# Optimization experiments

Hardware: AMD Instinct MI355X
Metric: run time of the kernel (lower is better)

## Reference

```python
import jax, jax.numpy as jnp
import numpy as np
import math

FEATURE_DIM = 512
QK_DIM = 256
EPS = 1e-12  # torch F.normalize eps


def _l2norm(x):
    n = jnp.linalg.norm(x, axis=-1, keepdims=True)
    return x / jnp.maximum(n, EPS)


def setup_inputs() -> dict:
    key = jax.random.key(0)
    ks = jax.random.split(key, 6)
    B, Nq, Nk = 16, 2048, 2048
    query = jax.random.normal(ks[0], (B, Nq, FEATURE_DIM), dtype=jnp.float32)
    key_t = jax.random.normal(ks[1], (B, Nk, FEATURE_DIM // 2), dtype=jnp.float32)
    value = jax.random.normal(ks[2], (B, Nk, FEATURE_DIM // 2), dtype=jnp.float32)
    # weights stored torch-style [out, in], init N(0, sqrt(2/out))
    WQ = jax.random.normal(ks[3], (QK_DIM, FEATURE_DIM), dtype=jnp.float32) * math.sqrt(2.0 / QK_DIM)
    WK = jax.random.normal(ks[4], (QK_DIM, FEATURE_DIM // 2), dtype=jnp.float32) * math.sqrt(2.0 / QK_DIM)
    WV = jax.random.normal(ks[5], (FEATURE_DIM, FEATURE_DIM // 2), dtype=jnp.float32) * math.sqrt(2.0 / FEATURE_DIM)
    return {"query": query, "key": key_t, "value": value, "WQ": WQ, "WK": WK, "WV": WV}


def reference(query, key, value, WQ, WK, WV):
    temp = QK_DIM ** (-0.5)
    w_q = _l2norm(jnp.einsum('bnf,qf->bnq', query, WQ))      # [B, Nq, D]
    w_k = _l2norm(jnp.einsum('bmf,qf->bmq', key, WK))        # [B, Nk, D]
    dot = jnp.einsum('bnd,bmd->bnm', w_q, w_k)               # cosine sims
    affinity = jax.nn.softmax(dot * temp, axis=-1)
    w_v = _l2norm(jnp.einsum('bmf,vf->bmv', value, WV))      # [B, Nk, F]
    out = jnp.einsum('bnm,bmv->bnv', affinity, w_v)
    return out + query
```

## Files before the change

### kernel.cpp

```cpp
#include <hip/hip_runtime.h>

typedef float        f32x4  __attribute__((ext_vector_type(4)));
typedef float        f32x16 __attribute__((ext_vector_type(16)));
typedef unsigned int u32x4  __attribute__((ext_vector_type(4)));
typedef unsigned int u32x2  __attribute__((ext_vector_type(2)));
typedef int          i32x2  __attribute__((ext_vector_type(2)));
typedef __bf16       bf16x8 __attribute__((ext_vector_type(8)));

#define DEVFN static __device__ __forceinline__

DEVFN unsigned cvtpk(float a, float b){
  unsigned r;
  asm("v_cvt_pk_bf16_f32 %0, %1, %2" : "=v"(r) : "v"(a), "v"(b));
  return r;
}
DEVFN float exp2_hw(float x){
  float r;
  asm("v_exp_f32 %0, %1" : "=v"(r) : "v"(x));
  return r;
}
DEVFN bf16x8 as_bf(u32x4 v){ union{u32x4 u; bf16x8 b;} x; x.u=v; return x.b; }

DEVFN unsigned char f2fp8(float v){
  int r = __builtin_amdgcn_cvt_pk_fp8_f32(v, v, 0, false);
  return (unsigned char)(r & 0xff);
}
DEVFN unsigned pk4_fp8(float a, float b, float c, float d){
  int r = __builtin_amdgcn_cvt_pk_fp8_f32(a, b, 0, false);
  r = __builtin_amdgcn_cvt_pk_fp8_f32(c, d, r, true);
  return (unsigned)r;
}
DEVFN long mk64(unsigned lo, unsigned hi){
  return (long)(((unsigned long long)hi << 32) | lo);
}

DEVFN void plswap(unsigned &x, unsigned &y, int h){
#if __has_builtin(__builtin_amdgcn_permlane32_swap)
  i32x2 r = __builtin_amdgcn_permlane32_swap((int)x, (int)y, false, false);
  x = (unsigned)r[0]; y = (unsigned)r[1];
#else
  unsigned ox = (unsigned)__shfl_xor((int)x, 32);
  unsigned oy = (unsigned)__shfl_xor((int)y, 32);
  unsigned nx = h ? oy : x;
  unsigned ny = h ? y  : ox;
  x = nx; y = ny;
#endif
}

DEVFN void gload16(const char* src, char* lds){
  __builtin_amdgcn_global_load_lds(
      (__attribute__((address_space(1))) void*)src,
      (__attribute__((address_space(3))) void*)lds, 16, 0, 0);
}

constexpr int BB = 16, NQ = 2048, NK = 2048, F = 512, D = 256, FV = 512;

template<int KD, int ND, int MODE>
__global__ __launch_bounds__(256,2) void proj_kernel(const float* __restrict__ X,
                                                     const float* __restrict__ W,
                                                     unsigned char* __restrict__ Y,
                                                     float scale)
{
  constexpr bool TR = (MODE == 2);
  constexpr int NW = ND/4;
  constexpr int AF = TR ? 8 : 2;
  constexpr int BF = TR ? 2 : NW/16;
  __shared__ __align__(16) char xsm[32*80];
  __shared__ __align__(16) char wsm[ND*80];
  __shared__ float wsum[4][32];
  const int tid = threadIdx.x;
  const int lane = tid & 63;
  const int wid = tid >> 6;
  const int q16 = lane & 15;
  const int g = lane >> 4;
  const int row0 = blockIdx.x * 32;
  const int rX = tid >> 3, cX = (tid & 7) * 4;

  f32x4 z4 = {0.f,0.f,0.f,0.f};
  f32x4 acc[AF][BF];
  #pragma unroll
  for (int i=0;i<AF;i++){
    #pragma unroll
    for (int j=0;j<BF;j++) acc[i][j] = z4;
  }

  f32x4 xr = *(const f32x4*)(X + (size_t)(row0+rX)*KD + cX);
  f32x4 wr[ND/32];
  #pragma unroll
  for (int j=0;j<ND/32;j++)
    wr[j] = *(const f32x4*)(W + (size_t)(j*32+rX)*KD + cX);

  for (int k0 = 0; k0 < KD; k0 += 32){
    {
      u32x2 p; p[0]=cvtpk(xr[0],xr[1]); p[1]=cvtpk(xr[2],xr[3]);
      *(u32x2*)(xsm + rX*80 + cX*2) = p;
    }
    #pragma unroll
    for (int j=0;j<ND/32;j++){
      u32x2 p; p[0]=cvtpk(wr[j][0],wr[j][1]); p[1]=cvtpk(wr[j][2],wr[j][3]);
      *(u32x2*)(wsm + (j*32+rX)*80 + cX*2) = p;
    }
    if (k0 + 32 < KD){
      xr = *(const f32x4*)(X + (size_t)(row0+rX)*KD + k0+32 + cX);
      #pragma unroll
      for (int j=0;j<ND/32;j++)
        wr[j] = *(const f32x4*)(W + (size_t)(j*32+rX)*KD + k0+32 + cX);
    }
    __syncthreads();
    if constexpr (!TR){
      bf16x8 a[2], bb[BF];
      #pragma unroll
      for (int mi=0;mi<2;mi++)  a[mi]  = as_bf(*(const u32x4*)(xsm + (16*mi+q16)*80 + g*16));
      #pragma unroll
      for (int ni=0;ni<BF;ni++) bb[ni] = as_bf(*(const u32x4*)(wsm + (wid*NW + 16*ni + q16)*80 + g*16));
      #pragma unroll
      for (int mi=0;mi<2;mi++){
        #pragma unroll
        for (int ni=0;ni<BF;ni++)
          acc[mi][ni] = __builtin_amdgcn_mfma_f32_16x16x32_bf16(a[mi], bb[ni], acc[mi][ni], 0,0,0);
      }
    } else {
      bf16x8 a[8], bb[2];
      #pragma unroll
      for (int ai=0;ai<8;ai++) a[ai] = as_bf(*(const u32x4*)(wsm + (wid*NW + 16*ai + q16)*80 + g*16));
      #pragma unroll
      for (int ci=0;ci<2;ci++) bb[ci] = as_bf(*(const u32x4*)(xsm + (16*ci+q16)*80 + g*16));
      #pragma unroll
      for (int ai=0;ai<8;ai++){
        #pragma unroll
        for (int ci=0;ci<2;ci++)
          acc[ai][ci] = __builtin_amdgcn_mfma_f32_16x16x32_bf16(a[ai], bb[ci], acc[ai][ci], 0,0,0);
      }
    }
    __syncthreads();
  }

  if constexpr (!TR){
    float part[2][4];
    #pragma unroll
    for (int mi=0;mi<2;mi++){
      #pragma unroll
      for (int r=0;r<4;r++){
        float s=0.f;
        #pragma unroll
        for (int ni=0;ni<BF;ni++){ float v=acc[mi][ni][r]; s += v*v; }
        part[mi][r]=s;
      }
    }
    #pragma unroll
    for (int m=1;m<16;m<<=1){
      #pragma unroll
      for (int mi=0;mi<2;mi++){
        #pragma unroll
        for (int r=0;r<4;r++) part[mi][r] += __shfl_xor(part[mi][r], m);
      }
    }
    if (q16 == 0){
      #pragma unroll
      for (int mi=0;mi<2;mi++){
        #pragma unroll
        for (int r=0;r<4;r++) wsum[wid][16*mi + 4*g + r] = part[mi][r];
      }
    }
    __syncthreads();
    #pragma unroll
    for (int mi=0;mi<2;mi++){
      #pragma unroll
      for (int r=0;r<4;r++){
        int m = 16*mi + 4*g + r;
        float tot = wsum[0][m]+wsum[1][m]+wsum[2][m]+wsum[3][m];
        float inv = scale / fmaxf(sqrtf(tot), 1e-12f);
        int row = row0 + m;
        #pragma unroll
        for (int ni=0;ni<BF;ni++){
          int col = wid*NW + 16*ni + q16;
          unsigned char vb = f2fp8(acc[mi][ni][r]*inv);
          if constexpr (MODE == 0){
            Y[(size_t)row*ND + col] = vb;
          } else {
            int b2 = row >> 11, kv = row & 2047;
            int kt = kv >> 5, mm = kv & 31;
            int u = col >> 5, dd = col & 31;
            int s = ((dd>>4)<<3) | (dd&7);
            int l = mm + ((dd>>3)&1)*32;
            Y[((((size_t)b2*64 + kt)*8 + u)*64 + l)*16 + s] = vb;
          }
        }
      }
    }
  } else {
    float pp[2];
    #pragma unroll
    for (int ci=0;ci<2;ci++){
      float s=0.f;
      #pragma unroll
      for (int ai=0;ai<8;ai++){
        #pragma unroll
        for (int r=0;r<4;r++){ float v=acc[ai][ci][r]; s += v*v; }
      }
      pp[ci]=s;
    }
    #pragma unroll
    for (int ci=0;ci<2;ci++){
      pp[ci] += __shfl_xor(pp[ci],16);
      pp[ci] += __shfl_xor(pp[ci],32);
    }
    if (lane < 16){ wsum[wid][lane] = pp[0]; wsum[wid][16+lane] = pp[1]; }
    __syncthreads();
    #pragma unroll
    for (int ci=0;ci<2;ci++){
      int m = 16*ci + q16;
      float tot = wsum[0][m]+wsum[1][m]+wsum[2][m]+wsum[3][m];
      float inv = scale / fmaxf(sqrtf(tot), 1e-12f);
      int grow = row0 + m;
      int b2 = grow >> 11;
      int kv = grow & 2047;
      int kt = kv >> 5, kl = kv & 31;
      int s = ((kl>>4)<<3) | (kl&7);
      int lofs = ((kl>>3)&1)*32;
      #pragma unroll
      for (int ai=0;ai<8;ai++){
        #pragma unroll
        for (int r=0;r<4;r++){
          int n = wid*NW + 16*ai + 4*g + r;
          int fvh = n >> 8, u = (n>>5)&7, mm = n & 31;
          unsigned char vb = f2fp8(acc[ai][ci][r]*inv);
          Y[(((((size_t)b2*64 + kt)*2 + fvh)*8 + u)*64 + (mm + lofs))*16 + s] = vb;
        }
      }
    }
  }
}

__global__ __launch_bounds__(256,2) void attn_kernel(const float* __restrict__ query,
    const unsigned char* __restrict__ wq8, const unsigned char* __restrict__ k8,
    const unsigned char* __restrict__ v8, float* __restrict__ out)
{
  __shared__ __align__(16) char smem[65536];
  const int tid = threadIdx.x, lane = tid & 63, wid = tid >> 6;
  const int l31 = lane & 31, h = lane >> 5;
  const int qs = wid & 1, fvh = wid >> 1;
  const int bid = blockIdx.x;
  const int lb = (bid & 7)*64 + (bid >> 3);
  const int b = lb >> 5;
  const int qblk = lb & 31;
  const int q0 = qblk*64;

  const char* ksrc = (const char*)(k8 + (size_t)b*524288)  + lane*16;
  const char* vsrc = (const char*)(v8 + (size_t)b*1048576) + lane*16;

  #define STAGE(T, CUR) do{                                                       \
    gload16(ksrc + (size_t)(T)*8192  +        wid*1024,                           \
            smem + (CUR)*8192 +        wid*1024);                                 \
    gload16(ksrc + (size_t)(T)*8192  + 4096 + wid*1024,                           \
            smem + (CUR)*8192 + 4096 + wid*1024);                                 \
    gload16(vsrc + (size_t)(T)*16384 +         wid*1024,                          \
            smem + 16384 + (CUR)*16384 +         wid*1024);                       \
    gload16(vsrc + (size_t)(T)*16384 +  4096 + wid*1024,                          \
            smem + 16384 + (CUR)*16384 +  4096 + wid*1024);                       \
    gload16(vsrc + (size_t)(T)*16384 +  8192 + wid*1024,                          \
            smem + 16384 + (CUR)*16384 +  8192 + wid*1024);                       \
    gload16(vsrc + (size_t)(T)*16384 + 12288 + wid*1024,                          \
            smem + 16384 + (CUR)*16384 + 12288 + wid*1024);                       \
  }while(0)

  STAGE(0, 0);

  unsigned long long qf[16];
  {
    const unsigned char* qb = wq8 + ((size_t)b*NQ + q0 + qs*32 + l31)*D;
    #pragma unroll
    for (int c=0;c<16;c++) qf[c] = *(const unsigned long long*)(qb + c*16 + h*8);
  }

  f32x16 z16;
  #pragma unroll
  for (int i=0;i<16;i++) z16[i]=0.f;
  f32x16 o[8];
  #pragma unroll
  for (int i=0;i<8;i++) o[i]=z16;
  float ssum = 0.f;
  const float c2 = 0.0625f * 1.4426950408889634f / 64.0f;

  __syncthreads();

  #define BODY(T, CUR) do{                                                          \
    if ((T) < 63) STAGE((T)+1, (CUR)^1);                                            \
    const char* kb = smem + (CUR)*8192;                                             \
    const char* vb = smem + 16384 + (CUR)*16384;                                    \
    f32x16 S = z16;                                                                 \
    __builtin_amdgcn_s_setprio(1);                                                  \
    _Pragma("unroll")                                                               \
    for (int u=0;u<8;u++){                                                          \
      u32x4 kk = *(const u32x4*)(kb + u*1024 + lane*16);                            \
      S = __builtin_amdgcn_mfma_f32_32x32x16_fp8_fp8(mk64(kk[0],kk[1]),             \
            (long)qf[2*u],   S, 0,0,0);                                             \
      S = __builtin_amdgcn_mfma_f32_32x32x16_fp8_fp8(mk64(kk[2],kk[3]),             \
            (long)qf[2*u+1], S, 0,0,0);                                             \
    }                                                                               \
    __builtin_amdgcn_s_setprio(0);                                                  \
    float p[16];                                                                    \
    _Pragma("unroll")                                                               \
    for (int r=0;r<16;r++) p[r] = exp2_hw(S[r]*c2);                                 \
    float s2[8];                                                                    \
    _Pragma("unroll")                                                               \
    for (int j=0;j<8;j++) s2[j] = p[2*j] + p[2*j+1];                                \
    float s4a = (s2[0]+s2[1]) + (s2[2]+s2[3]);                                      \
    float s4b = (s2[4]+s2[5]) + (s2[6]+s2[7]);                                      \
    ssum += s4a + s4b;                                                              \
    unsigned d0 = pk4_fp8(p[0],p[1],p[2],p[3]);                   \
    unsigned d1 = pk4_fp8(p[4],p[5],p[6],p[7]);                   \
    unsigned d2 = pk4_fp8(p[8],p[9],p[10],p[11]);                 \
    unsigned d3 = pk4_fp8(p[12],p[13],p[14],p[15]);               \
    plswap(d0, d1, h);  plswap(d2, d3, h);                                          \
    long P0 = mk64(d0, d1);                               \
    long P1 = mk64(d2, d3);                               \
    __builtin_amdgcn_s_setprio(1);                                                  \
    _Pragma("unroll")                                                               \
    for (int u=0;u<8;u++){                                                          \
      u32x4 vv = *(const u32x4*)(vb + (fvh*8+u)*1024 + lane*16);                    \
      o[u] = __builtin_amdgcn_mfma_f32_32x32x16_fp8_fp8(mk64(vv[0],vv[1]), P0,      \
                                                        o[u], 0,0,0);               \
      o[u] = __builtin_amdgcn_mfma_f32_32x32x16_fp8_fp8(mk64(vv[2],vv[3]), P1,      \
                                                        o[u], 0,0,0);               \
    }                                                                               \
    __builtin_amdgcn_s_setprio(0);                                                  \
    __syncthreads();                                                                \
  }while(0)

  for (int tt = 0; tt < 64; tt += 2){
    BODY(tt,   0);
    BODY(tt+1, 1);
  }
  #undef BODY
  #undef STAGE

  ssum += __shfl_xor(ssum, 32);
  const float inv = 1.f/(8.f*ssum);
  #pragma unroll
  for (int i=0;i<8;i++){
    #pragma unroll
    for (int r=0;r<16;r++) o[i][r] *= inv;
  }

  char* wsc = smem + qs*16384;
  union U16 { f32x16 v; f32x4 q4[4]; };
  const int swz = (l31 & 7) << 4;
  #pragma unroll
  for (int phase=0; phase<2; ++phase){
    if (fvh == phase){
      #pragma unroll
      for (int hf=0; hf<2; ++hf){
        #pragma unroll
        for (int fc2=0; fc2<4; ++fc2){
          U16 u; u.v = o[hf*4+fc2];
          #pragma unroll
          for (int k=0;k<4;k++){
            *(f32x4*)(wsc + l31*512 + ((fc2*128 + k*32 + h*16) ^ swz)) = u.q4[k];
          }
        }
        #pragma unroll
        for (int p2=0;p2<16;p2++){
          int qr = p2*2 + h;
          f32x4 v = *(const f32x4*)(wsc + qr*512 + ((l31*16) ^ ((qr&7)<<4)));
          size_t row = (size_t)b*NQ + q0 + qs*32 + qr;
          int col = fvh*256 + hf*128 + l31*4;
          f32x4 qv = *(const f32x4*)(query + row*F + col);
          #pragma unroll
          for (int e=0;e<4;e++) v[e] += qv[e];
          *(f32x4*)(out + row*F + col) = v;
        }
      }
    }
    __syncthreads();
  }
}

extern "C" void kernel_launch(void* const* d_in, const int* in_sizes, int n_in,
                              void* d_out, int out_size, void* d_ws, size_t ws_size,
                              hipStream_t stream)
{
  const float* query = (const float*)d_in[0];
  const float* key   = (const float*)d_in[1];
  const float* value = (const float*)d_in[2];
  const float* WQ    = (const float*)d_in[3];
  const float* WK    = (const float*)d_in[4];
  const float* WV    = (const float*)d_in[5];
  float* out = (float*)d_out;

  unsigned char* wq8 = (unsigned char*)d_ws;
  unsigned char* k8  = wq8 + (size_t)BB*NQ*D;
  unsigned char* v8  = k8  + (size_t)BB*NK*D;

  dim3 blk(256);
  proj_kernel<512,256,0><<<1024, blk, 0, stream>>>(query, WQ, wq8, 8.0f);
  proj_kernel<256,256,1><<<1024, blk, 0, stream>>>(key,   WK, k8,  8.0f);
  proj_kernel<256,512,2><<<1024, blk, 0, stream>>>(value, WV, v8,  8.0f);
  attn_kernel<<<512, blk, 0, stream>>>(query, wq8, k8, v8, out);
}
```

Measured before the change: 189.2 us.

## Switch attention to 32x32x64 scaled fp8 MFMA with 512-thread blocks and LDS P exchange

Replaces the 32x32x16 fp8 MFMAs with the gfx950 scaled 32x32x64 f8f6f4 MFMA, which needs a K/V layout in the projection kernels that packs 64-deep k-chunks per lane. Each attention block now has 8 waves covering 128 queries over 64-key tiles, and the keys are split between wave pairs. The softmax probabilities are exchanged through LDS instead of permlane swaps, with an extra barrier, and row sums are combined across the wave pair at the end. The aim is to halve the MFMA instruction count and reuse each staged K/V tile across more queries. The cost is more LDS, an extra sync per tile, and fewer, larger blocks.

Result: slower. 272.7 us (+44.1%).

```diff
diff --git a/kernel.cpp b/kernel.cpp
--- a/kernel.cpp
+++ b/kernel.cpp
@@ -5,6 +5,7 @@
 typedef unsigned int u32x4  __attribute__((ext_vector_type(4)));
 typedef unsigned int u32x2  __attribute__((ext_vector_type(2)));
 typedef int          i32x2  __attribute__((ext_vector_type(2)));
+typedef int          i32x8  __attribute__((ext_vector_type(8)));
 typedef __bf16       bf16x8 __attribute__((ext_vector_type(8)));
 
 #define DEVFN static __device__ __forceinline__
@@ -30,21 +31,11 @@
   r = __builtin_amdgcn_cvt_pk_fp8_f32(c, d, r, true);
   return (unsigned)r;
 }
-DEVFN long mk64(unsigned lo, unsigned hi){
-  return (long)(((unsigned long long)hi << 32) | lo);
-}
-
-DEVFN void plswap(unsigned &x, unsigned &y, int h){
-#if __has_builtin(__builtin_amdgcn_permlane32_swap)
-  i32x2 r = __builtin_amdgcn_permlane32_swap((int)x, (int)y, false, false);
-  x = (unsigned)r[0]; y = (unsigned)r[1];
-#else
-  unsigned ox = (unsigned)__shfl_xor((int)x, 32);
-  unsigned oy = (unsigned)__shfl_xor((int)y, 32);
-  unsigned nx = h ? oy : x;
-  unsigned ny = h ? y  : ox;
-  x = nx; y = ny;
-#endif
+DEVFN i32x8 mk8(u32x4 lo, u32x4 hi){
+  i32x8 r;
+  r[0]=(int)lo[0]; r[1]=(int)lo[1]; r[2]=(int)lo[2]; r[3]=(int)lo[3];
+  r[4]=(int)hi[0]; r[5]=(int)hi[1]; r[6]=(int)hi[2]; r[7]=(int)hi[3];
+  return r;
 }
 
 DEVFN void gload16(const char* src, char* lds){
@@ -54,6 +45,7 @@
 }
 
 constexpr int BB = 16, NQ = 2048, NK = 2048, F = 512, D = 256, FV = 512;
+#define SC1 0x7f7f7f7f
 
 template<int KD, int ND, int MODE>
 __global__ __launch_bounds__(256,2) void proj_kernel(const float* __restrict__ X,
@@ -179,11 +171,10 @@
             Y[(size_t)row*ND + col] = vb;
           } else {
             int b2 = row >> 11, kv = row & 2047;
-            int kt = kv >> 5, mm = kv & 31;
-            int u = col >> 5, dd = col & 31;
-            int s = ((dd>>4)<<3) | (dd&7);
-            int l = mm + ((dd>>3)&1)*32;
-            Y[((((size_t)b2*64 + kt)*8 + u)*64 + l)*16 + s] = vb;
+            int kt = kv >> 5, l31k = kv & 31;
+            int u = col >> 6, hh = (col >> 5) & 1, j = col & 31;
+            Y[(((size_t)b2*64 + kt)*4 + u)*2048 + (j>>4)*1024
+              + (l31k + 32*hh)*16 + (j&15)] = vb;
           }
         }
       }
@@ -215,62 +206,65 @@
       int grow = row0 + m;
       int b2 = grow >> 11;
       int kv = grow & 2047;
-      int kt = kv >> 5, kl = kv & 31;
-      int s = ((kl>>4)<<3) | (kl&7);
-      int lofs = ((kl>>3)&1)*32;
+      int t64 = kv >> 6, hh = (kv >> 5) & 1, j = kv & 31;
       #pragma unroll
       for (int ai=0;ai<8;ai++){
         #pragma unroll
         for (int r=0;r<4;r++){
           int n = wid*NW + 16*ai + 4*g + r;
-          int fvh = n >> 8, u = (n>>5)&7, mm = n & 31;
+          int fvb = n >> 5, l31v = n & 31;
           unsigned char vb = f2fp8(acc[ai][ci][r]*inv);
-          Y[(((((size_t)b2*64 + kt)*2 + fvh)*8 + u)*64 + (mm + lofs))*16 + s] = vb;
+          Y[(((size_t)b2*32 + t64)*16 + fvb)*2048 + (j>>4)*1024
+            + (l31v + 32*hh)*16 + (j&15)] = vb;
         }
       }
     }
   }
 }
 
-__global__ __launch_bounds__(256,2) void attn_kernel(const float* __restrict__ query,
+__global__ __launch_bounds__(512,2) void attn_kernel(const float* __restrict__ query,
     const unsigned char* __restrict__ wq8, const unsigned char* __restrict__ k8,
     const unsigned char* __restrict__ v8, float* __restrict__ out)
 {
-  __shared__ __align__(16) char smem[65536];
+  __shared__ __align__(16) char smem[106496];
   const int tid = threadIdx.x, lane = tid & 63, wid = tid >> 6;
   const int l31 = lane & 31, h = lane >> 5;
-  const int qs = wid & 1, fvh = wid >> 1;
+  const int qs = wid & 3, fvh = wid >> 2;
   const int bid = blockIdx.x;
-  const int lb = (bid & 7)*64 + (bid >> 3);
-  const int b = lb >> 5;
-  const int qblk = lb & 31;
-  const int q0 = qblk*64;
+  const int lb = (bid & 7)*32 + (bid >> 3);
+  const int b = lb >> 4;
+  const int qblk = lb & 15;
+  const int q0 = qblk*128;
 
   const char* ksrc = (const char*)(k8 + (size_t)b*524288)  + lane*16;
   const char* vsrc = (const char*)(v8 + (size_t)b*1048576) + lane*16;
-
-  #define STAGE(T, CUR) do{                                                       \
-    gload16(ksrc + (size_t)(T)*8192  +        wid*1024,                           \
-            smem + (CUR)*8192 +        wid*1024);                                 \
-    gload16(ksrc + (size_t)(T)*8192  + 4096 + wid*1024,                           \
-            smem + (CUR)*8192 + 4096 + wid*1024);                                 \
-    gload16(vsrc + (size_t)(T)*16384 +         wid*1024,                          \
-            smem + 16384 + (CUR)*16384 +         wid*1024);                       \
-    gload16(vsrc + (size_t)(T)*16384 +  4096 + wid*1024,                          \
-            smem + 16384 + (CUR)*16384 +  4096 + wid*1024);                       \
-    gload16(vsrc + (size_t)(T)*16384 +  8192 + wid*1024,                          \
-            smem + 16384 + (CUR)*16384 +  8192 + wid*1024);                       \
-    gload16(vsrc + (size_t)(T)*16384 + 12288 + wid*1024,                          \
-            smem + 16384 + (CUR)*16384 + 12288 + wid*1024);                       \
+  char* const pbase = smem + 98304;
+
+  #define STAGE_K(T, CUR) do{                                                \
+    gload16(ksrc + (size_t)(T)*16384 + (2*wid  )*1024,                       \
+            smem + (CUR)*16384 + (2*wid  )*1024);                            \
+    gload16(ksrc + (size_t)(T)*16384 + (2*wid+1)*1024,                       \
+            smem + (CUR)*16384 + (2*wid+1)*1024);                            \
   }while(0)
-
-  STAGE(0, 0);
-
-  unsigned long long qf[16];
+  #define STAGE_V(T, CUR) do{                                                \
+    _Pragma("unroll")                                                        \
+    for (int i_=0;i_<4;i_++)                                                 \
+      gload16(vsrc + (size_t)(T)*32768 + (4*wid+i_)*1024,                    \
+              smem + 32768 + (CUR)*32768 + (4*wid+i_)*1024);                 \
+  }while(0)
+
+  STAGE_K(0, 0);
+  STAGE_V(0, 0);
+
+  i32x8 qf[4];
   {
     const unsigned char* qb = wq8 + ((size_t)b*NQ + q0 + qs*32 + l31)*D;
     #pragma unroll
-    for (int c=0;c<16;c++) qf[c] = *(const unsigned long long*)(qb + c*16 + h*8);
+    for (int u=0;u<4;u++){
+      u32x4 lo = *(const u32x4*)(qb + u*64 + h*32);
+      u32x4 hi = *(const u32x4*)(qb + u*64 + h*32 + 16);
+      qf[u] = mk8(lo, hi);
+    }
   }
 
   f32x16 z16;
@@ -285,57 +279,66 @@
   __syncthreads();
 
   #define BODY(T, CUR) do{                                                          \
-    if ((T) < 63) STAGE((T)+1, (CUR)^1);                                            \
-    const char* kb = smem + (CUR)*8192;                                             \
-    const char* vb = smem + 16384 + (CUR)*16384;                                    \
+    if ((T) < 31) STAGE_K((T)+1, (CUR)^1);                                          \
+    const char* kb = smem + (CUR)*16384 + fvh*8192;                                 \
     f32x16 S = z16;                                                                 \
     __builtin_amdgcn_s_setprio(1);                                                  \
     _Pragma("unroll")                                                               \
-    for (int u=0;u<8;u++){                                                          \
-      u32x4 kk = *(const u32x4*)(kb + u*1024 + lane*16);                            \
-      S = __builtin_amdgcn_mfma_f32_32x32x16_fp8_fp8(mk64(kk[0],kk[1]),             \
-            (long)qf[2*u],   S, 0,0,0);                                             \
-      S = __builtin_amdgcn_mfma_f32_32x32x16_fp8_fp8(mk64(kk[2],kk[3]),             \
-            (long)qf[2*u+1], S, 0,0,0);                                             \
+    for (int u=0;u<4;u++){                                                          \
+      u32x4 alo = *(const u32x4*)(kb + u*2048 +        lane*16);                    \
+      u32x4 ahi = *(const u32x4*)(kb + u*2048 + 1024 + lane*16);                    \
+      S = __builtin_amdgcn_mfma_scale_f32_32x32x64_f8f6f4(                          \
+            mk8(alo,ahi), qf[u], S, 0, 0, 0, SC1, 0, SC1);                          \
     }                                                                               \
     __builtin_amdgcn_s_setprio(0);                                                  \
     float p[16];                                                                    \
     _Pragma("unroll")                                                               \
     for (int r=0;r<16;r++) p[r] = exp2_hw(S[r]*c2);                                 \
-    float s2[8];                                                                    \
-    _Pragma("unroll")                                                               \
-    for (int j=0;j<8;j++) s2[j] = p[2*j] + p[2*j+1];                                \
-    float s4a = (s2[0]+s2[1]) + (s2[2]+s2[3]);                                      \
-    float s4b = (s2[4]+s2[5]) + (s2[6]+s2[7]);                                      \
-    ssum += s4a + s4b;                                                              \
-    unsigned d0 = pk4_fp8(p[0],p[1],p[2],p[3]);                   \
-    unsigned d1 = pk4_fp8(p[4],p[5],p[6],p[7]);                   \
-    unsigned d2 = pk4_fp8(p[8],p[9],p[10],p[11]);                 \
-    unsigned d3 = pk4_fp8(p[12],p[13],p[14],p[15]);               \
-    plswap(d0, d1, h);  plswap(d2, d3, h);                                          \
-    long P0 = mk64(d0, d1);                               \
-    long P1 = mk64(d2, d3);                               \
+    {                                                                               \
+      float s2a = (p[0]+p[1])+(p[2]+p[3]),  s2b = (p[4]+p[5])+(p[6]+p[7]);          \
+      float s2c = (p[8]+p[9])+(p[10]+p[11]), s2d = (p[12]+p[13])+(p[14]+p[15]);     \
+      ssum += (s2a+s2b) + (s2c+s2d);                                                \
+    }                                                                               \
+    {                                                                               \
+      u32x4 pw = { pk4_fp8(p[0],p[1],p[2],p[3]),   pk4_fp8(p[4],p[5],p[6],p[7]),    \
+                   pk4_fp8(p[8],p[9],p[10],p[11]), pk4_fp8(p[12],p[13],p[14],p[15])};\
+      *(u32x4*)(pbase + ((qs*2+fvh)*2 + h)*512 + l31*16) = pw;                      \
+    }                                                                               \
+    __syncthreads();                                    \
+    if ((T) < 31) STAGE_V((T)+1, (CUR)^1);                                          \
+    u32x4 r0 = *(const u32x4*)(pbase + ((qs*2+h)*2    )*512 + l31*16);              \
+    u32x4 r1 = *(const u32x4*)(pbase + ((qs*2+h)*2 + 1)*512 + l31*16);              \
+    i32x8 pb;                                                                       \
+    pb[0]=(int)r0[0]; pb[1]=(int)r1[0]; pb[2]=(int)r0[1]; pb[3]=(int)r1[1];         \
+    pb[4]=(int)r0[2]; pb[5]=(int)r1[2]; pb[6]=(int)r0[3]; pb[7]=(int)r1[3];         \
+    const char* vb = smem + 32768 + (CUR)*32768 + fvh*16384;                        \
     __builtin_amdgcn_s_setprio(1);                                                  \
     _Pragma("unroll")                                                               \
     for (int u=0;u<8;u++){                                                          \
-      u32x4 vv = *(const u32x4*)(vb + (fvh*8+u)*1024 + lane*16);                    \
-      o[u] = __builtin_amdgcn_mfma_f32_32x32x16_fp8_fp8(mk64(vv[0],vv[1]), P0,      \
-                                                        o[u], 0,0,0);               \
-      o[u] = __builtin_amdgcn_mfma_f32_32x32x16_fp8_fp8(mk64(vv[2],vv[3]), P1,      \
-                                                        o[u], 0,0,0);               \
+      u32x4 vlo = *(const u32x4*)(vb + u*2048 +        lane*16);                    \
+      u32x4 vhi = *(const u32x4*)(vb + u*2048 + 1024 + lane*16);                    \
+      o[u] = __builtin_amdgcn_mfma_scale_f32_32x32x64_f8f6f4(                       \
+               mk8(vlo,vhi), pb, o[u], 0, 0, 0, SC1, 0, SC1);                       \
     }                                                                               \
     __builtin_amdgcn_s_setprio(0);                                                  \
-    __syncthreads();                                                                \
+    __syncthreads();                                              \
   }while(0)
 
-  for (int tt = 0; tt < 64; tt += 2){
+  for (int tt = 0; tt < 32; tt += 2){
     BODY(tt,   0);
     BODY(tt+1, 1);
   }
   #undef BODY
-  #undef STAGE
+  #undef STAGE_K
+  #undef STAGE_V
 
   ssum += __shfl_xor(ssum, 32);
+  {
+    float* sx = (float*)pbase;
+    sx[(qs*2+fvh)*32 + l31] = ssum;
+    __syncthreads();
+    ssum += sx[(qs*2+(1-fvh))*32 + l31];
+  }
   const float inv = 1.f/(8.f*ssum);
   #pragma unroll
   for (int i=0;i<8;i++){
@@ -396,5 +399,5 @@
   proj_kernel<512,256,0><<<1024, blk, 0, stream>>>(query, WQ, wq8, 8.0f);
   proj_kernel<256,256,1><<<1024, blk, 0, stream>>>(key,   WK, k8,  8.0f);
   proj_kernel<256,512,2><<<1024, blk, 0, stream>>>(value, WV, v8,  8.0f);
-  attn_kernel<<<512, blk, 0, stream>>>(query, wq8, k8, v8, out);
-}
+  attn_kernel<<<256, dim3(512), 0, stream>>>(query, wq8, k8, v8, out);
+}
```
